# Performance work log

Measured on AMD Instinct MI355X. Metric: run time of the kernel, lower is better.

Reference implementation:

```python
import jax, jax.numpy as jnp
import numpy as np

T, S, B, D, H, FFN = 1024, 1024, 4, 1024, 16, 4096
HD = D // H
EPS = 1e-5


def xavier(key, shape, gain=1.0):
    fan_out, fan_in = shape
    a = gain * np.sqrt(6.0 / (fan_in + fan_out))
    return jax.random.uniform(key, shape, jnp.float32, -a, a)


def layer_norm(x, g, b):
    mu = jnp.mean(x, axis=-1, keepdims=True)
    var = jnp.mean(jnp.square(x - mu), axis=-1, keepdims=True)
    return (x - mu) / jnp.sqrt(var + EPS) * g + b


def mha(q, k, v, Wq, bq, Wk, bk, Wv, bv, Wo, bo, key_padding_mask=None, attn_mask=None):
    # q: [t,b,d]; k,v: [s,b,d]; key_padding_mask: [b,s] bool (True = pad)
    t, b, d = q.shape
    s = v.shape[0]
    if key_padding_mask is not None:
        # original zeroes the KEY tensor before projection
        k = k * (~key_padding_mask).T[:, :, None]
    Q = (q @ Wq.T + bq).reshape(t, b, H, HD)
    K = (k @ Wk.T + bk).reshape(s, b, H, HD)
    V = (v @ Wv.T + bv).reshape(s, b, H, HD)
    scores = jnp.einsum('tbhk,sbhk->bhts', Q, K) / jnp.sqrt(jnp.float32(HD))
    if attn_mask is not None:
        scores = scores + attn_mask  # additive [t,s] broadcast over b,h
    p = jax.nn.softmax(scores, axis=-1)
    ctx = jnp.einsum('bhts,sbhk->tbhk', p, V)  # [t,b,h,hd]
    out = ctx.reshape(t, b, d)
    attn_w = jnp.swapaxes(ctx, 0, 2)  # [h,b,t,hd] as in original
    return out @ Wo.T + bo, attn_w


def setup_inputs() -> dict:
    key = jax.random.key(0)
    ks = jax.random.split(key, 16)
    inv2 = 1.0 / np.sqrt(2.0)
    d = {
        'state': jax.random.normal(ks[0], (T, B, D), jnp.float32),
        'encoder_out': jax.random.normal(ks[1], (S, B, D), jnp.float32),
        'self_attn_mask': jnp.triu(jnp.full((T, T), -1e9, jnp.float32), 1),
        'self_attn_padding_mask': jnp.zeros((B, T), bool),
        'encoder_padding_mask': jnp.broadcast_to(jnp.arange(S)[None, :] >= (S - S // 10), (B, S)),
        # self-attention projections
        'sa_Wq': xavier(ks[2], (D, D), inv2), 'sa_bq': jnp.zeros((D,), jnp.float32),
        'sa_Wk': xavier(ks[3], (D, D), inv2), 'sa_bk': jnp.zeros((D,), jnp.float32),
        'sa_Wv': xavier(ks[4], (D, D), inv2), 'sa_bv': jnp.zeros((D,), jnp.float32),
        'sa_Wo': xavier(ks[5], (D, D)), 'sa_bo': jnp.zeros((D,), jnp.float32),
        # encoder-decoder attention projections
        'ea_Wq': xavier(ks[6], (D, D), inv2), 'ea_bq': jnp.zeros((D,), jnp.float32),
        'ea_Wk': xavier(ks[7], (D, D), inv2), 'ea_bk': jnp.zeros((D,), jnp.float32),
        'ea_Wv': xavier(ks[8], (D, D), inv2), 'ea_bv': jnp.zeros((D,), jnp.float32),
        'ea_Wo': xavier(ks[9], (D, D)), 'ea_bo': jnp.zeros((D,), jnp.float32),
        # layernorms
        'ln1_g': jnp.ones((D,), jnp.float32), 'ln1_b': jnp.zeros((D,), jnp.float32),
        'ln2_g': jnp.ones((D,), jnp.float32), 'ln2_b': jnp.zeros((D,), jnp.float32),
        'ln3_g': jnp.ones((D,), jnp.float32), 'ln3_b': jnp.zeros((D,), jnp.float32),
        # FFN
        'fc1_W': xavier(ks[10], (FFN, D)), 'fc1_b': jnp.zeros((FFN,), jnp.float32),
        'fc2_W': xavier(ks[11], (D, FFN)), 'fc2_b': jnp.zeros((D,), jnp.float32),
    }
    return d


def reference(state, encoder_out, self_attn_mask, self_attn_padding_mask, encoder_padding_mask,
              sa_Wq, sa_bq, sa_Wk, sa_bk, sa_Wv, sa_bv, sa_Wo, sa_bo,
              ea_Wq, ea_bq, ea_Wk, ea_bk, ea_Wv, ea_bv, ea_Wo, ea_bo,
              ln1_g, ln1_b, ln2_g, ln2_b, ln3_g, ln3_b,
              fc1_W, fc1_b, fc2_W, fc2_b):
    x = state
    # self-attention block (dropout is identity in eval)
    res = x
    a, _ = mha(x, x, x, sa_Wq, sa_bq, sa_Wk, sa_bk, sa_Wv, sa_bv, sa_Wo, sa_bo,
               key_padding_mask=self_attn_padding_mask, attn_mask=self_attn_mask)
    x = layer_norm(a + res, ln1_g, ln1_b)
    # encoder-decoder attention block
    res = x
    a, attn = mha(x, encoder_out, encoder_out, ea_Wq, ea_bq, ea_Wk, ea_bk, ea_Wv, ea_bv, ea_Wo, ea_bo,
                  key_padding_mask=encoder_padding_mask, attn_mask=None)
    x = layer_norm(a + res, ln2_g, ln2_b)
    # FFN block
    res = x
    h = jax.nn.relu(x @ fc1_W.T + fc1_b)
    x = layer_norm(h @ fc2_W.T + fc2_b + res, ln3_g, ln3_b)
    return (x, attn)
```

## Files before the change

kernel.cpp:

```cpp
#include <hip/hip_runtime.h>
#include <hip/hip_bf16.h>


typedef __attribute__((ext_vector_type(8))) short bf16x8;
typedef __attribute__((ext_vector_type(4))) float f32x4;
typedef __attribute__((ext_vector_type(8))) unsigned short us8;
typedef __attribute__((ext_vector_type(4))) unsigned short us4;

#define AS1 __attribute__((address_space(1)))
#define AS3 __attribute__((address_space(3)))

#define T_LEN 1024
#define S_LEN 1024
#define B_DIM 4
#define D_MOD 1024
#define H_NUM 16
#define FFN_D 4096
#define NTOK  4096

__device__ __forceinline__ float b2f(unsigned short u) {
    return __uint_as_float(((unsigned int)u) << 16);
}
__device__ __forceinline__ unsigned short f2b(float f) {
    unsigned int x = __float_as_uint(f);
    x += 0x7fffu + ((x >> 16) & 1u);
    return (unsigned short)(x >> 16);
}

struct CvtArgs {
    const float* s[12];
    unsigned short* d[12];
};

__global__ __launch_bounds__(256) void cvt_all_kernel(CvtArgs a)
{
    const int cnt[12] = {2048, 2048, 512, 512, 512, 512, 512, 512, 512, 512, 2048, 2048};
    int bid = blockIdx.x;
    int seg = 0;
    while (bid >= cnt[seg]) { bid -= cnt[seg]; ++seg; }
    const size_t off = (size_t)bid * 2048 + threadIdx.x * 8;
    const float* src = a.s[seg] + off;
    unsigned short* dst = a.d[seg] + off;
    const f32x4 v0 = *(const f32x4*)src;
    const f32x4 v1 = *(const f32x4*)(src + 4);
    us8 o;
#pragma unroll
    for (int j = 0; j < 4; ++j) { o[j] = f2b(v0[j]); o[4 + j] = f2b(v1[j]); }
    *(us8*)dst = o;
}

template <int BN>
__global__ __launch_bounds__(512, 1) void gemm8ph_kernel(
    const unsigned short* __restrict__ A,
    const unsigned short* __restrict__ W,
    const float* __restrict__ b0, const float* __restrict__ b1,
    const float* __restrict__ b2, const float* __restrict__ b3,
    const int* __restrict__ rowmask, unsigned int maskbits,
    unsigned short* __restrict__ p0, unsigned short* __restrict__ p1,
    unsigned short* __restrict__ p2, unsigned short* __restrict__ p3,
    int ostride,
    const float* __restrict__ resid, float* __restrict__ outf,
    float* __restrict__ partf,
    int M, int N, int K, int relu, int ksplit)
{
    constexpr int NR  = BN / 64;
    constexpr int BLH = (BN * 64) / 8192;
    constexpr int BBUF = BN * 128;

    __shared__ __align__(16) char ldsb[65536 + 2 * BBUF];

    const int tid  = threadIdx.x;
    const int lane = tid & 63;
    const int wid  = tid >> 6;
    const int wr   = wid >> 2;
    const int wc   = wid & 3;
    const int row0 = blockIdx.x * 256;
    const int col0 = blockIdx.y * BN;
    const int rsel = lane & 15;
    const int kg2  = (lane >> 4) * 16;
    const int kz   = blockIdx.z;
    const int Keff = K / ksplit;
    const int koff = kz * Keff;
    const int NT   = Keff >> 6;

    f32x4 acc[8][NR];
#pragma unroll
    for (int m = 0; m < 8; ++m)
#pragma unroll
        for (int n = 0; n < NR; ++n)
            acc[m][n] = (f32x4){0.f, 0.f, 0.f, 0.f};

    auto stageA = [&](int buf, int half, int t) {
        const int k0 = koff + (t << 6);
#pragma unroll
        for (int i = 0; i < 2; ++i) {
            const unsigned int beta = (unsigned int)(half * 16384 + i * 8192 + tid * 16);
            const unsigned int lam  = beta ^ (((beta >> 7) & 7u) << 4);
            const char* src = (const char*)A +
                ((size_t)(row0 + (int)(lam >> 7)) * K + k0) * 2 + (lam & 127u);
            __builtin_amdgcn_global_load_lds((const AS1 void*)src,
                (AS3 void*)(ldsb + buf * 32768 + beta), 16, 0, 0);
        }
    };
    auto stageB = [&](int buf, int half, int t) {
        const int k0 = koff + (t << 6);
#pragma unroll
        for (int i = 0; i < BLH; ++i) {
            const unsigned int beta = (unsigned int)(half * (BN * 64) + i * 8192 + tid * 16);
            const unsigned int lam  = beta ^ (((beta >> 7) & 7u) << 4);
            const char* src = (const char*)W +
                ((size_t)(col0 + (int)(lam >> 7)) * K + k0) * 2 + (lam & 127u);
            __builtin_amdgcn_global_load_lds((const AS1 void*)src,
                (AS3 void*)(ldsb + 65536 + buf * BBUF + beta), 16, 0, 0);
        }
    };
    auto readA = [&](int buf, int m, int k) -> bf16x8 {
        const int r = wr * 128 + m * 16 + rsel;
        const unsigned int l  = (unsigned int)(r * 128 + k * 64 + kg2);
        const unsigned int ph = l ^ (((unsigned int)(r & 7)) << 4);
        return *(const bf16x8*)(ldsb + buf * 32768 + ph);
    };
    auto readB = [&](int buf, int n, int k) -> bf16x8 {
        const int r = wc * (BN / 4) + n * 16 + rsel;
        const unsigned int l  = (unsigned int)(r * 128 + k * 64 + kg2);
        const unsigned int ph = l ^ (((unsigned int)(r & 7)) << 4);
        return *(const bf16x8*)(ldsb + 65536 + buf * BBUF + ph);
    };

    stageA(0, 0, 0); stageA(0, 1, 0); stageB(0, 0, 0); stageB(0, 1, 0);
    stageA(1, 0, 1); stageA(1, 1, 1);
    asm volatile("s_waitcnt vmcnt(4)" ::: "memory");
    __builtin_amdgcn_s_barrier();

    bf16x8 Afr[8][2], Bfr[NR][2];

    for (int t = 0; t < NT; ++t) {
        const int cur = t & 1;
#pragma unroll
        for (int m = 0; m < 4; ++m) { Afr[m][0] = readA(cur, m, 0); Afr[m][1] = readA(cur, m, 1); }
#pragma unroll
        for (int n = 0; n < NR; ++n) Bfr[n][0] = readB(cur, n, 0);
        if (t + 1 < NT) stageB(cur ^ 1, 0, t + 1);
        __builtin_amdgcn_s_barrier();
        asm volatile("s_waitcnt lgkmcnt(0)" ::: "memory");
        __builtin_amdgcn_sched_barrier(0);
        __builtin_amdgcn_s_setprio(1);
#pragma unroll
        for (int m = 0; m < 4; ++m)
#pragma unroll
            for (int n = 0; n < NR; ++n)
                acc[m][n] = __builtin_amdgcn_mfma_f32_16x16x32_bf16(Afr[m][0], Bfr[n][0], acc[m][n], 0, 0, 0);
        __builtin_amdgcn_s_setprio(0);
        __builtin_amdgcn_s_barrier();
#pragma unroll
        for (int m = 4; m < 8; ++m) { Afr[m][0] = readA(cur, m, 0); Afr[m][1] = readA(cur, m, 1); }
#pragma unroll
        for (int n = 0; n < NR; ++n) Bfr[n][1] = readB(cur, n, 1);
        if (t + 1 < NT) stageB(cur ^ 1, 1, t + 1);
        __builtin_amdgcn_s_barrier();
        asm volatile("s_waitcnt lgkmcnt(0)" ::: "memory");
        __builtin_amdgcn_sched_barrier(0);
        __builtin_amdgcn_s_setprio(1);
#pragma unroll
        for (int m = 4; m < 8; ++m)
#pragma unroll
            for (int n = 0; n < NR; ++n)
                acc[m][n] = __builtin_amdgcn_mfma_f32_16x16x32_bf16(Afr[m][0], Bfr[n][0], acc[m][n], 0, 0, 0);
        __builtin_amdgcn_s_setprio(0);
        __builtin_amdgcn_s_barrier();
        if (t + 2 < NT) stageA(cur, 0, t + 2);
        __builtin_amdgcn_s_barrier();
        __builtin_amdgcn_s_setprio(1);
#pragma unroll
        for (int m = 0; m < 4; ++m)
#pragma unroll
            for (int n = 0; n < NR; ++n)
                acc[m][n] = __builtin_amdgcn_mfma_f32_16x16x32_bf16(Afr[m][1], Bfr[n][1], acc[m][n], 0, 0, 0);
        __builtin_amdgcn_s_setprio(0);
        __builtin_amdgcn_s_barrier();
        if (t + 2 < NT) stageA(cur, 1, t + 2);
        __builtin_amdgcn_s_barrier();
        __builtin_amdgcn_s_setprio(1);
#pragma unroll
        for (int m = 4; m < 8; ++m)
#pragma unroll
            for (int n = 0; n < NR; ++n)
                acc[m][n] = __builtin_amdgcn_mfma_f32_16x16x32_bf16(Afr[m][1], Bfr[n][1], acc[m][n], 0, 0, 0);
        __builtin_amdgcn_s_setprio(0);
        if (t + 2 < NT) { asm volatile("s_waitcnt vmcnt(4)" ::: "memory"); }
        else            { asm volatile("s_waitcnt vmcnt(0)" ::: "memory"); }
        __builtin_amdgcn_s_barrier();
    }

    const int seq  = M >> 2;
    const int c    = col0 >> 10;
    unsigned short* op = c == 0 ? p0 : c == 1 ? p1 : c == 2 ? p2 : p3;
    const float*    bp = c == 0 ? b0 : c == 1 ? b1 : c == 2 ? b2 : b3;
    const bool um = rowmask && ((maskbits >> c) & 1u);
    const int rbas = (lane >> 4) * 4;
    if (partf && kz > 0) {
#pragma unroll
        for (int m = 0; m < 8; ++m)
#pragma unroll
            for (int n = 0; n < NR; ++n)
#pragma unroll
                for (int j = 0; j < 4; ++j) {
                    const int gr = row0 + wr * 128 + m * 16 + rbas + j;
                    const int gc = col0 + wc * (BN / 4) + n * 16 + rsel;
                    partf[(size_t)gr * N + gc] = acc[m][n][j];
                }
    } else {
#pragma unroll
        for (int m = 0; m < 8; ++m)
#pragma unroll
            for (int n = 0; n < NR; ++n)
#pragma unroll
                for (int j = 0; j < 4; ++j) {
                    const int gr = row0 + wr * 128 + m * 16 + rbas + j;
                    const int gc = col0 + wc * (BN / 4) + n * 16 + rsel;
                    float v = acc[m][n][j];
                    if (um && rowmask[(gr & 3) * seq + (gr >> 2)] != 0) v = 0.f;
                    v += bp[gc & 1023];
                    if (relu) v = fmaxf(v, 0.f);
                    if (resid) v += resid[(size_t)gr * N + gc];
                    if (outf) outf[(size_t)gr * N + gc] = v;
                    else      op[(size_t)gr * ostride + (gc & 1023)] = f2b(v);
                }
    }
}

__global__ __launch_bounds__(256) void vtrans_kernel(
    const unsigned short* __restrict__ Vb, unsigned short* __restrict__ Vt)
{
    __shared__ unsigned short tile[64 * 72];
    const int tid = threadIdx.x;
    const int t0  = blockIdx.x * 64;
    const int bh  = blockIdx.y;
    const int h   = bh & (H_NUM - 1);
    const int b   = bh >> 4;

    const int r   = tid >> 2;
    const int c16 = (tid & 3) * 16;
    const unsigned short* src = Vb + ((size_t)(t0 + r) * B_DIM + b) * D_MOD + h * 64 + c16;
    *(us8*)&tile[r * 72 + c16]     = *(const us8*)src;
    *(us8*)&tile[r * 72 + c16 + 8] = *(const us8*)(src + 8);
    __syncthreads();

    const int dr  = tid >> 2;
    const int tch = (tid & 3) * 16;
    us8 o0, o1;
#pragma unroll
    for (int j = 0; j < 8; ++j) {
        o0[j] = tile[(tch + j) * 72 + dr];
        o1[j] = tile[(tch + 8 + j) * 72 + dr];
    }
    unsigned short* dst = Vt + (size_t)(bh * 64 + dr) * S_LEN + t0 + tch;
    *(us8*)dst       = o0;
    *(us8*)(dst + 8) = o1;
}

__global__ __launch_bounds__(256, 3) void flash_mfma_kernel(
    const unsigned short* __restrict__ Qb,
    const unsigned short* __restrict__ Kb,
    const unsigned short* __restrict__ Vt,
    unsigned short* __restrict__ outc,
    float* __restrict__ outp,
    int causal)
{
    __shared__ __align__(16) unsigned short Ks[2][64 * 64];
    __shared__ __align__(16) unsigned short Vts[2][64 * 64];
    __shared__ __align__(16) unsigned short Ps[4][16 * 72];

    const int tid  = threadIdx.x;
    const int lane = tid & 63;
    const int wv   = tid >> 6;
    const int g    = lane >> 4;
    const int n    = lane & 15;
    const int t0   = blockIdx.x * 64;
    const int bh   = blockIdx.y;
    const int h    = bh & (H_NUM - 1);
    const int b    = bh >> 4;
    const int woff = wv * 16;

    bf16x8 qa[2];
    {
        const unsigned short* qptr =
            Qb + ((size_t)(t0 + woff + n) * B_DIM + b) * D_MOD + h * 64 + g * 8;
        qa[0] = *(const bf16x8*)qptr;
        qa[1] = *(const bf16x8*)(qptr + 32);
    }

    f32x4 ctx[4];
#pragma unroll
    for (int nt = 0; nt < 4; ++nt) ctx[nt] = (f32x4){0.f, 0.f, 0.f, 0.f};
    float m_run[4], l_run[4];
#pragma unroll
    for (int j = 0; j < 4; ++j) { m_run[j] = -INFINITY; l_run[j] = 0.f; }

    unsigned short* pw = &Ps[wv][0];
    const int smax = causal ? (t0 + 64) : S_LEN;
    const int NTt  = smax >> 6;

    auto stage = [&](int buf, int s0) {
#pragma unroll
        for (int i = 0; i < 2; ++i) {
            const unsigned int beta = (unsigned int)(i * 4096 + tid * 16);
            const unsigned int lam  = beta ^ (((beta >> 7) & 7u) << 4);
            const int row = (int)(lam >> 7);
            const unsigned int colb = lam & 127u;
            const char* srcK = (const char*)Kb +
                ((size_t)((s0 + row) * B_DIM + b) * D_MOD + h * 64) * 2 + colb;
            __builtin_amdgcn_global_load_lds((const AS1 void*)srcK,
                (AS3 void*)((char*)&Ks[buf][0] + beta), 16, 0, 0);
            const char* srcV = (const char*)Vt +
                ((size_t)(bh * 64 + row) * S_LEN + s0) * 2 + colb;
            __builtin_amdgcn_global_load_lds((const AS1 void*)srcV,
                (AS3 void*)((char*)&Vts[buf][0] + beta), 16, 0, 0);
        }
    };

    stage(0, 0);
    for (int t = 0; t < NTt; ++t) {
        const int s0  = t << 6;
        const int cur = t & 1;
        asm volatile("s_waitcnt vmcnt(0)" ::: "memory");
        __builtin_amdgcn_s_barrier();
        if (t + 1 < NTt) stage(cur ^ 1, s0 + 64);

        f32x4 sacc[4];
#pragma unroll
        for (int u = 0; u < 4; ++u) sacc[u] = (f32x4){0.f, 0.f, 0.f, 0.f};
#pragma unroll
        for (int u = 0; u < 4; ++u) {
#pragma unroll
            for (int kc = 0; kc < 2; ++kc) {
                const int r = u * 16 + n;
                const unsigned int l  = (unsigned int)(r * 128 + kc * 64 + g * 16);
                const unsigned int ph = l ^ (((unsigned int)(r & 7)) << 4);
                const bf16x8 kb = *(const bf16x8*)((const char*)&Ks[cur][0] + ph);
                sacc[u] = __builtin_amdgcn_mfma_f32_16x16x32_bf16(qa[kc], kb, sacc[u], 0, 0, 0);
            }
        }

        const bool diag = causal && (s0 + 64 > t0);
        float scj[4];
#pragma unroll
        for (int j = 0; j < 4; ++j) {
            float p[4];
#pragma unroll
            for (int u = 0; u < 4; ++u) p[u] = sacc[u][j] * 0.125f;
            if (diag) {
                const int tq = t0 + woff + g * 4 + j;
#pragma unroll
                for (int u = 0; u < 4; ++u)
                    if (s0 + u * 16 + n > tq) p[u] += -1e9f;
            }
            float pm = fmaxf(fmaxf(p[0], p[1]), fmaxf(p[2], p[3]));
            pm = fmaxf(pm, __shfl_xor(pm, 1));
            pm = fmaxf(pm, __shfl_xor(pm, 2));
            pm = fmaxf(pm, __shfl_xor(pm, 4));
            pm = fmaxf(pm, __shfl_xor(pm, 8));
            const float m_new = fmaxf(m_run[j], pm);
            const float sc = __expf(m_run[j] - m_new);
            m_run[j] = m_new;
            float e[4];
#pragma unroll
            for (int u = 0; u < 4; ++u) e[u] = __expf(p[u] - m_new);
            float ls = (e[0] + e[1]) + (e[2] + e[3]);
            ls += __shfl_xor(ls, 1);
            ls += __shfl_xor(ls, 2);
            ls += __shfl_xor(ls, 4);
            ls += __shfl_xor(ls, 8);
            l_run[j] = l_run[j] * sc + ls;
            scj[j] = sc;
#pragma unroll
            for (int u = 0; u < 4; ++u)
                pw[(g * 4 + j) * 72 + u * 16 + n] = f2b(e[u]);
        }
#pragma unroll
        for (int nt = 0; nt < 4; ++nt)
#pragma unroll
            for (int j = 0; j < 4; ++j) ctx[nt][j] *= scj[j];

        bf16x8 pa[2];
#pragma unroll
        for (int ks = 0; ks < 2; ++ks)
            pa[ks] = *(const bf16x8*)&pw[n * 72 + ks * 32 + g * 8];
#pragma unroll
        for (int nt = 0; nt < 4; ++nt) {
#pragma unroll
            for (int ks = 0; ks < 2; ++ks) {
                const int r = nt * 16 + n;
                const unsigned int l  = (unsigned int)(r * 128 + ks * 64 + g * 16);
                const unsigned int ph = l ^ (((unsigned int)(r & 7)) << 4);
                const bf16x8 vb = *(const bf16x8*)((const char*)&Vts[cur][0] + ph);
                ctx[nt] = __builtin_amdgcn_mfma_f32_16x16x32_bf16(pa[ks], vb, ctx[nt], 0, 0, 0);
            }
        }
    }

    float inv[4];
#pragma unroll
    for (int j = 0; j < 4; ++j) inv[j] = 1.f / l_run[j];
#pragma unroll
    for (int nt = 0; nt < 4; ++nt) {
#pragma unroll
        for (int j = 0; j < 4; ++j) {
            const int t = t0 + woff + g * 4 + j;
            const int d = nt * 16 + n;
            const float v = ctx[nt][j] * inv[j];
            outc[((size_t)t * B_DIM + b) * D_MOD + h * 64 + d] = f2b(v);
            if (outp)
                outp[((size_t)(h * B_DIM + b) * T_LEN + t) * 64 + d] = v;
        }
    }
}

__global__ __launch_bounds__(256) void layernorm_kernel(
    const float* __restrict__ y,
    const float* __restrict__ part,
    const float* __restrict__ g,
    const float* __restrict__ be,
    float* __restrict__ out_f,
    unsigned short* __restrict__ out_bf)
{
    __shared__ float red[8];
    const int row = blockIdx.x;
    const int tid = threadIdx.x;
    f32x4 v = *(const f32x4*)&y[(size_t)row * D_MOD + tid * 4];
    if (part) {
        const f32x4 pv = *(const f32x4*)&part[(size_t)row * D_MOD + tid * 4];
#pragma unroll
        for (int j = 0; j < 4; ++j) v[j] += pv[j];
    }
    float s = v[0] + v[1] + v[2] + v[3];
#pragma unroll
    for (int o = 32; o > 0; o >>= 1) s += __shfl_xor(s, o);
    if ((tid & 63) == 0) red[tid >> 6] = s;
    __syncthreads();
    const float mu = (red[0] + red[1] + red[2] + red[3]) * (1.f / D_MOD);
    const float d0 = v[0] - mu, d1 = v[1] - mu, d2 = v[2] - mu, d3 = v[3] - mu;
    float s2 = d0 * d0 + d1 * d1 + d2 * d2 + d3 * d3;
#pragma unroll
    for (int o = 32; o > 0; o >>= 1) s2 += __shfl_xor(s2, o);
    if ((tid & 63) == 0) red[4 + (tid >> 6)] = s2;
    __syncthreads();
    const float var  = (red[4] + red[5] + red[6] + red[7]) * (1.f / D_MOD);
    const float rstd = rsqrtf(var + 1e-5f);
    const float dd[4] = {d0, d1, d2, d3};
    f32x4 of;
    us4 ob;
#pragma unroll
    for (int j = 0; j < 4; ++j) {
        const int col = tid * 4 + j;
        const float r = dd[j] * rstd * g[col] + be[col];
        of[j] = r;
        ob[j] = f2b(r);
    }
    const size_t oi = (size_t)row * D_MOD + tid * 4;
    if (out_f)  *(f32x4*)&out_f[oi] = of;
    if (out_bf) *(us4*)&out_bf[oi]  = ob;
}

extern "C" void kernel_launch(void* const* d_in, const int* in_sizes, int n_in,
                              void* d_out, int out_size, void* d_ws, size_t ws_size,
                              hipStream_t stream) {
    (void)in_sizes; (void)n_in; (void)out_size; (void)ws_size;

    const float* x0    = (const float*)d_in[0];
    const float* enc   = (const float*)d_in[1];
    const int* sa_pad  = (const int*)d_in[3];
    const int* ea_pad  = (const int*)d_in[4];
    const float* sa_Wq = (const float*)d_in[5];
    const float* sa_bq = (const float*)d_in[6];
    const float* sa_Wk = (const float*)d_in[7];
    const float* sa_bk = (const float*)d_in[8];
    const float* sa_Wv = (const float*)d_in[9];
    const float* sa_bv = (const float*)d_in[10];
    const float* sa_Wo = (const float*)d_in[11];
    const float* sa_bo = (const float*)d_in[12];
    const float* ea_Wq = (const float*)d_in[13];
    const float* ea_bq = (const float*)d_in[14];
    const float* ea_Wk = (const float*)d_in[15];
    const float* ea_bk = (const float*)d_in[16];
    const float* ea_Wv = (const float*)d_in[17];
    const float* ea_bv = (const float*)d_in[18];
    const float* ea_Wo = (const float*)d_in[19];
    const float* ea_bo = (const float*)d_in[20];
    const float* ln1_g = (const float*)d_in[21];
    const float* ln1_b = (const float*)d_in[22];
    const float* ln2_g = (const float*)d_in[23];
    const float* ln2_b = (const float*)d_in[24];
    const float* ln3_g = (const float*)d_in[25];
    const float* ln3_b = (const float*)d_in[26];
    const float* fc1_W = (const float*)d_in[27];
    const float* fc1_b = (const float*)d_in[28];
    const float* fc2_W = (const float*)d_in[29];
    const float* fc2_b = (const float*)d_in[30];

    const size_t DD = (size_t)D_MOD * D_MOD;
    const size_t FD = (size_t)FFN_D * D_MOD;
    const size_t SL = (size_t)NTOK * D_MOD;

    unsigned short* ws_us = (unsigned short*)d_ws;
    unsigned short* wb[10];
    for (int i = 0; i < 8; ++i) wb[i] = ws_us + i * DD;
    wb[8] = ws_us + 8 * DD;
    wb[9] = ws_us + 8 * DD + FD;
    unsigned short* abf = ws_us + 8 * DD + 2 * FD;
    unsigned short* ebf = abf + SL;
    unsigned short* Cb  = ebf + SL;
    unsigned short* Qb  = Cb + SL;
    unsigned short* Kb  = Qb + SL;
    unsigned short* Vb  = Kb + SL;
    unsigned short* Vt  = Vb + SL;
    unsigned short* Hbf = Qb;
    float* fbase = (float*)(Vt + SL);
    float* Yf  = fbase;
    float* X1f = fbase + SL;
    float* Pq  = (float*)Qb;
    float* Pa  = (float*)abf;

    float* outx = (float*)d_out;
    float* outa = outx + SL;

    const dim3 blk(256);
    const dim3 blk512(512);
    const dim3 g_attn(T_LEN / 64, B_DIM * H_NUM);
    unsigned short* nbf = nullptr;
    float* nff = nullptr;
    const float* nf = nullptr;
    const int* ni = nullptr;

    {
        CvtArgs ca;
        const float* srcs[12]  = {x0, enc, sa_Wq, sa_Wk, sa_Wv, sa_Wo,
                                  ea_Wq, ea_Wk, ea_Wv, ea_Wo, fc1_W, fc2_W};
        unsigned short* dsts[12] = {abf, ebf, wb[0], wb[1], wb[2], wb[3],
                                    wb[4], wb[5], wb[6], wb[7], wb[8], wb[9]};
        for (int i = 0; i < 12; ++i) { ca.s[i] = srcs[i]; ca.d[i] = dsts[i]; }
        cvt_all_kernel<<<dim3(12288), blk, 0, stream>>>(ca);
    }

    gemm8ph_kernel<256><<<dim3(16, 12, 1), blk512, 0, stream>>>(
        abf, wb[0], sa_bq, sa_bk, sa_bv, sa_bv, sa_pad, 0x2u,
        Qb, Kb, Vb, Vb, D_MOD, nf, nff, nff, NTOK, 3072, D_MOD, 0, 1);
    vtrans_kernel<<<g_attn, blk, 0, stream>>>(Vb, Vt);
    flash_mfma_kernel<<<g_attn, blk, 0, stream>>>(Qb, Kb, Vt, Cb, nff, 1);
    gemm8ph_kernel<128><<<dim3(16, 8, 2), blk512, 0, stream>>>(
        Cb, wb[3], sa_bo, sa_bo, sa_bo, sa_bo, ni, 0u,
        nbf, nbf, nbf, nbf, D_MOD, x0, Yf, Pq, NTOK, D_MOD, D_MOD, 0, 2);
    layernorm_kernel<<<dim3(NTOK), blk, 0, stream>>>(Yf, Pq, ln1_g, ln1_b, X1f, abf);

    gemm8ph_kernel<128><<<dim3(16, 8, 1), blk512, 0, stream>>>(
        abf, wb[4], ea_bq, ea_bq, ea_bq, ea_bq, ni, 0u,
        Qb, Qb, Qb, Qb, D_MOD, nf, nff, nff, NTOK, D_MOD, D_MOD, 0, 1);
    gemm8ph_kernel<128><<<dim3(16, 16, 1), blk512, 0, stream>>>(
        ebf, wb[5], ea_bk, ea_bv, ea_bv, ea_bv, ea_pad, 0x1u,
        Kb, Vb, Vb, Vb, D_MOD, nf, nff, nff, NTOK, 2048, D_MOD, 0, 1);
    vtrans_kernel<<<g_attn, blk, 0, stream>>>(Vb, Vt);
    flash_mfma_kernel<<<g_attn, blk, 0, stream>>>(Qb, Kb, Vt, Cb, outa, 0);
    gemm8ph_kernel<128><<<dim3(16, 8, 2), blk512, 0, stream>>>(
        Cb, wb[7], ea_bo, ea_bo, ea_bo, ea_bo, ni, 0u,
        nbf, nbf, nbf, nbf, D_MOD, X1f, Yf, Pq, NTOK, D_MOD, D_MOD, 0, 2);
    layernorm_kernel<<<dim3(NTOK), blk, 0, stream>>>(Yf, Pq, ln2_g, ln2_b, X1f, ebf);

    gemm8ph_kernel<256><<<dim3(16, 16, 1), blk512, 0, stream>>>(
        ebf, wb[8], fc1_b, fc1_b + 1024, fc1_b + 2048, fc1_b + 3072, ni, 0u,
        Hbf, Hbf + 1024, Hbf + 2048, Hbf + 3072, FFN_D, nf, nff, nff,
        NTOK, FFN_D, D_MOD, 1, 1);
    gemm8ph_kernel<128><<<dim3(16, 8, 2), blk512, 0, stream>>>(
        Hbf, wb[9], fc2_b, fc2_b, fc2_b, fc2_b, ni, 0u,
        nbf, nbf, nbf, nbf, D_MOD, X1f, Yf, Pa, NTOK, D_MOD, FFN_D, 0, 2);
    layernorm_kernel<<<dim3(NTOK), blk, 0, stream>>>(Yf, Pa, ln3_g, ln3_b, outx, nbf);
}
```

Before: 683.6 us.

## Transpose flash-attention score MFMA, simplify softmax reductions, add NR=2 GEMM schedule

```diff
diff --git a/kernel.cpp b/kernel.cpp
--- a/kernel.cpp
+++ b/kernel.cpp
@@ -132,64 +132,102 @@
     asm volatile("s_waitcnt vmcnt(4)" ::: "memory");
     __builtin_amdgcn_s_barrier();
 
-    bf16x8 Afr[8][2], Bfr[NR][2];
-
-    for (int t = 0; t < NT; ++t) {
-        const int cur = t & 1;
-#pragma unroll
-        for (int m = 0; m < 4; ++m) { Afr[m][0] = readA(cur, m, 0); Afr[m][1] = readA(cur, m, 1); }
-#pragma unroll
-        for (int n = 0; n < NR; ++n) Bfr[n][0] = readB(cur, n, 0);
-        if (t + 1 < NT) stageB(cur ^ 1, 0, t + 1);
-        __builtin_amdgcn_s_barrier();
-        asm volatile("s_waitcnt lgkmcnt(0)" ::: "memory");
-        __builtin_amdgcn_sched_barrier(0);
-        __builtin_amdgcn_s_setprio(1);
-#pragma unroll
-        for (int m = 0; m < 4; ++m)
-#pragma unroll
-            for (int n = 0; n < NR; ++n)
-                acc[m][n] = __builtin_amdgcn_mfma_f32_16x16x32_bf16(Afr[m][0], Bfr[n][0], acc[m][n], 0, 0, 0);
-        __builtin_amdgcn_s_setprio(0);
-        __builtin_amdgcn_s_barrier();
-#pragma unroll
-        for (int m = 4; m < 8; ++m) { Afr[m][0] = readA(cur, m, 0); Afr[m][1] = readA(cur, m, 1); }
-#pragma unroll
-        for (int n = 0; n < NR; ++n) Bfr[n][1] = readB(cur, n, 1);
-        if (t + 1 < NT) stageB(cur ^ 1, 1, t + 1);
-        __builtin_amdgcn_s_barrier();
-        asm volatile("s_waitcnt lgkmcnt(0)" ::: "memory");
-        __builtin_amdgcn_sched_barrier(0);
-        __builtin_amdgcn_s_setprio(1);
-#pragma unroll
-        for (int m = 4; m < 8; ++m)
-#pragma unroll
-            for (int n = 0; n < NR; ++n)
-                acc[m][n] = __builtin_amdgcn_mfma_f32_16x16x32_bf16(Afr[m][0], Bfr[n][0], acc[m][n], 0, 0, 0);
-        __builtin_amdgcn_s_setprio(0);
-        __builtin_amdgcn_s_barrier();
-        if (t + 2 < NT) stageA(cur, 0, t + 2);
-        __builtin_amdgcn_s_barrier();
-        __builtin_amdgcn_s_setprio(1);
-#pragma unroll
-        for (int m = 0; m < 4; ++m)
-#pragma unroll
-            for (int n = 0; n < NR; ++n)
-                acc[m][n] = __builtin_amdgcn_mfma_f32_16x16x32_bf16(Afr[m][1], Bfr[n][1], acc[m][n], 0, 0, 0);
-        __builtin_amdgcn_s_setprio(0);
-        __builtin_amdgcn_s_barrier();
-        if (t + 2 < NT) stageA(cur, 1, t + 2);
-        __builtin_amdgcn_s_barrier();
-        __builtin_amdgcn_s_setprio(1);
-#pragma unroll
-        for (int m = 4; m < 8; ++m)
-#pragma unroll
-            for (int n = 0; n < NR; ++n)
-                acc[m][n] = __builtin_amdgcn_mfma_f32_16x16x32_bf16(Afr[m][1], Bfr[n][1], acc[m][n], 0, 0, 0);
-        __builtin_amdgcn_s_setprio(0);
-        if (t + 2 < NT) { asm volatile("s_waitcnt vmcnt(4)" ::: "memory"); }
-        else            { asm volatile("s_waitcnt vmcnt(0)" ::: "memory"); }
-        __builtin_amdgcn_s_barrier();
+    if constexpr (NR == 2) {
+        bf16x8 Af[8][2], Bf[2][2];
+        for (int t = 0; t < NT; ++t) {
+            const int cur = t & 1;
+#pragma unroll
+            for (int m = 0; m < 8; ++m) { Af[m][0] = readA(cur, m, 0); Af[m][1] = readA(cur, m, 1); }
+#pragma unroll
+            for (int n = 0; n < 2; ++n) Bf[n][0] = readB(cur, n, 0);
+            if (t + 1 < NT) { stageB(cur ^ 1, 0, t + 1); stageB(cur ^ 1, 1, t + 1); }
+            __builtin_amdgcn_s_barrier();
+            asm volatile("s_waitcnt lgkmcnt(0)" ::: "memory");
+            __builtin_amdgcn_sched_barrier(0);
+            __builtin_amdgcn_s_setprio(1);
+#pragma unroll
+            for (int m = 0; m < 8; ++m)
+#pragma unroll
+                for (int n = 0; n < 2; ++n)
+                    acc[m][n] = __builtin_amdgcn_mfma_f32_16x16x32_bf16(Af[m][0], Bf[n][0], acc[m][n], 0, 0, 0);
+            __builtin_amdgcn_s_setprio(0);
+            __builtin_amdgcn_s_barrier();
+#pragma unroll
+            for (int n = 0; n < 2; ++n) Bf[n][1] = readB(cur, n, 1);
+            if (t + 2 < NT) { stageA(cur, 0, t + 2); stageA(cur, 1, t + 2); }
+            __builtin_amdgcn_s_barrier();
+            asm volatile("s_waitcnt lgkmcnt(0)" ::: "memory");
+            __builtin_amdgcn_sched_barrier(0);
+            __builtin_amdgcn_s_setprio(1);
+#pragma unroll
+            for (int m = 0; m < 8; ++m)
+#pragma unroll
+                for (int n = 0; n < 2; ++n)
+                    acc[m][n] = __builtin_amdgcn_mfma_f32_16x16x32_bf16(Af[m][1], Bf[n][1], acc[m][n], 0, 0, 0);
+            __builtin_amdgcn_s_setprio(0);
+            if (t + 2 < NT) { asm volatile("s_waitcnt vmcnt(4)" ::: "memory"); }
+            else            { asm volatile("s_waitcnt vmcnt(0)" ::: "memory"); }
+            __builtin_amdgcn_s_barrier();
+        }
+    } else {
+        bf16x8 Afr[8][2], Bfr[NR][2];
+        for (int t = 0; t < NT; ++t) {
+            const int cur = t & 1;
+#pragma unroll
+            for (int m = 0; m < 4; ++m) { Afr[m][0] = readA(cur, m, 0); Afr[m][1] = readA(cur, m, 1); }
+#pragma unroll
+            for (int n = 0; n < NR; ++n) Bfr[n][0] = readB(cur, n, 0);
+            if (t + 1 < NT) stageB(cur ^ 1, 0, t + 1);
+            __builtin_amdgcn_s_barrier();
+            asm volatile("s_waitcnt lgkmcnt(0)" ::: "memory");
+            __builtin_amdgcn_sched_barrier(0);
+            __builtin_amdgcn_s_setprio(1);
+#pragma unroll
+            for (int m = 0; m < 4; ++m)
+#pragma unroll
+                for (int n = 0; n < NR; ++n)
+                    acc[m][n] = __builtin_amdgcn_mfma_f32_16x16x32_bf16(Afr[m][0], Bfr[n][0], acc[m][n], 0, 0, 0);
+            __builtin_amdgcn_s_setprio(0);
+            __builtin_amdgcn_s_barrier();
+#pragma unroll
+            for (int m = 4; m < 8; ++m) { Afr[m][0] = readA(cur, m, 0); Afr[m][1] = readA(cur, m, 1); }
+#pragma unroll
+            for (int n = 0; n < NR; ++n) Bfr[n][1] = readB(cur, n, 1);
+            if (t + 1 < NT) stageB(cur ^ 1, 1, t + 1);
+            __builtin_amdgcn_s_barrier();
+            asm volatile("s_waitcnt lgkmcnt(0)" ::: "memory");
+            __builtin_amdgcn_sched_barrier(0);
+            __builtin_amdgcn_s_setprio(1);
+#pragma unroll
+            for (int m = 4; m < 8; ++m)
+#pragma unroll
+                for (int n = 0; n < NR; ++n)
+                    acc[m][n] = __builtin_amdgcn_mfma_f32_16x16x32_bf16(Afr[m][0], Bfr[n][0], acc[m][n], 0, 0, 0);
+            __builtin_amdgcn_s_setprio(0);
+            __builtin_amdgcn_s_barrier();
+            if (t + 2 < NT) stageA(cur, 0, t + 2);
+            __builtin_amdgcn_s_barrier();
+            __builtin_amdgcn_s_setprio(1);
+#pragma unroll
+            for (int m = 0; m < 4; ++m)
+#pragma unroll
+                for (int n = 0; n < NR; ++n)
+                    acc[m][n] = __builtin_amdgcn_mfma_f32_16x16x32_bf16(Afr[m][1], Bfr[n][1], acc[m][n], 0, 0, 0);
+            __builtin_amdgcn_s_setprio(0);
+            __builtin_amdgcn_s_barrier();
+            if (t + 2 < NT) stageA(cur, 1, t + 2);
+            __builtin_amdgcn_s_barrier();
+            __builtin_amdgcn_s_setprio(1);
+#pragma unroll
+            for (int m = 4; m < 8; ++m)
+#pragma unroll
+                for (int n = 0; n < NR; ++n)
+                    acc[m][n] = __builtin_amdgcn_mfma_f32_16x16x32_bf16(Afr[m][1], Bfr[n][1], acc[m][n], 0, 0, 0);
+            __builtin_amdgcn_s_setprio(0);
+            if (t + 2 < NT) { asm volatile("s_waitcnt vmcnt(4)" ::: "memory"); }
+            else            { asm volatile("s_waitcnt vmcnt(0)" ::: "memory"); }
+            __builtin_amdgcn_s_barrier();
+        }
     }
 
     const int seq  = M >> 2;
@@ -234,8 +272,8 @@
 {
     __shared__ unsigned short tile[64 * 72];
     const int tid = threadIdx.x;
-    const int t0  = blockIdx.x * 64;
-    const int bh  = blockIdx.y;
+    const int bh  = blockIdx.x;
+    const int t0  = blockIdx.y * 64;
     const int h   = bh & (H_NUM - 1);
     const int b   = bh >> 4;
 
@@ -276,8 +314,9 @@
     const int wv   = tid >> 6;
     const int g    = lane >> 4;
     const int n    = lane & 15;
-    const int t0   = blockIdx.x * 64;
-    const int bh   = blockIdx.y;
+    const int g4   = g * 4;
+    const int bh   = blockIdx.x;
+    const int t0   = blockIdx.y * 64;
     const int h    = bh & (H_NUM - 1);
     const int b    = bh >> 4;
     const int woff = wv * 16;
@@ -293,13 +332,12 @@
     f32x4 ctx[4];
 #pragma unroll
     for (int nt = 0; nt < 4; ++nt) ctx[nt] = (f32x4){0.f, 0.f, 0.f, 0.f};
-    float m_run[4], l_run[4];
-#pragma unroll
-    for (int j = 0; j < 4; ++j) { m_run[j] = -INFINITY; l_run[j] = 0.f; }
+    float m_run = -INFINITY, l_run = 0.f;
 
     unsigned short* pw = &Ps[wv][0];
     const int smax = causal ? (t0 + 64) : S_LEN;
     const int NTt  = smax >> 6;
+    const int tq   = t0 + woff + n;
 
     auto stage = [&](int buf, int s0) {
 #pragma unroll
@@ -338,49 +376,51 @@
                 const unsigned int l  = (unsigned int)(r * 128 + kc * 64 + g * 16);
                 const unsigned int ph = l ^ (((unsigned int)(r & 7)) << 4);
                 const bf16x8 kb = *(const bf16x8*)((const char*)&Ks[cur][0] + ph);
-                sacc[u] = __builtin_amdgcn_mfma_f32_16x16x32_bf16(qa[kc], kb, sacc[u], 0, 0, 0);
+                sacc[u] = __builtin_amdgcn_mfma_f32_16x16x32_bf16(kb, qa[kc], sacc[u], 0, 0, 0);
             }
         }
 
         const bool diag = causal && (s0 + 64 > t0);
-        float scj[4];
-#pragma unroll
-        for (int j = 0; j < 4; ++j) {
-            float p[4];
-#pragma unroll
-            for (int u = 0; u < 4; ++u) p[u] = sacc[u][j] * 0.125f;
-            if (diag) {
-                const int tq = t0 + woff + g * 4 + j;
-#pragma unroll
-                for (int u = 0; u < 4; ++u)
-                    if (s0 + u * 16 + n > tq) p[u] += -1e9f;
+        float pv[4][4];
+        float pm = -INFINITY;
+#pragma unroll
+        for (int u = 0; u < 4; ++u)
+#pragma unroll
+            for (int j = 0; j < 4; ++j) {
+                float p = sacc[u][j] * 0.125f;
+                if (diag && (s0 + u * 16 + g4 + j > tq)) p += -1e9f;
+                pv[u][j] = p;
+                pm = fmaxf(pm, p);
             }
-            float pm = fmaxf(fmaxf(p[0], p[1]), fmaxf(p[2], p[3]));
-            pm = fmaxf(pm, __shfl_xor(pm, 1));
-            pm = fmaxf(pm, __shfl_xor(pm, 2));
-            pm = fmaxf(pm, __shfl_xor(pm, 4));
-            pm = fmaxf(pm, __shfl_xor(pm, 8));
-            const float m_new = fmaxf(m_run[j], pm);
-            const float sc = __expf(m_run[j] - m_new);
-            m_run[j] = m_new;
-            float e[4];
-#pragma unroll
-            for (int u = 0; u < 4; ++u) e[u] = __expf(p[u] - m_new);
-            float ls = (e[0] + e[1]) + (e[2] + e[3]);
-            ls += __shfl_xor(ls, 1);
-            ls += __shfl_xor(ls, 2);
-            ls += __shfl_xor(ls, 4);
-            ls += __shfl_xor(ls, 8);
-            l_run[j] = l_run[j] * sc + ls;
-            scj[j] = sc;
-#pragma unroll
-            for (int u = 0; u < 4; ++u)
-                pw[(g * 4 + j) * 72 + u * 16 + n] = f2b(e[u]);
-        }
+        pm = fmaxf(pm, __shfl_xor(pm, 16));
+        pm = fmaxf(pm, __shfl_xor(pm, 32));
+        const float m_new = fmaxf(m_run, pm);
+        const float sc = __expf(m_run - m_new);
+        m_run = m_new;
+        float ls = 0.f;
+#pragma unroll
+        for (int u = 0; u < 4; ++u) {
+            const float e0 = __expf(pv[u][0] - m_new);
+            const float e1 = __expf(pv[u][1] - m_new);
+            const float e2 = __expf(pv[u][2] - m_new);
+            const float e3 = __expf(pv[u][3] - m_new);
+            ls += (e0 + e1) + (e2 + e3);
+            const unsigned int w0 = (unsigned int)f2b(e0) | ((unsigned int)f2b(e1) << 16);
+            const unsigned int w1 = (unsigned int)f2b(e2) | ((unsigned int)f2b(e3) << 16);
+            *(unsigned int*)&pw[n * 72 + u * 16 + g4]     = w0;
+            *(unsigned int*)&pw[n * 72 + u * 16 + g4 + 2] = w1;
+        }
+        ls += __shfl_xor(ls, 16);
+        ls += __shfl_xor(ls, 32);
+        l_run = l_run * sc + ls;
+
+        float scq[4];
+#pragma unroll
+        for (int j = 0; j < 4; ++j) scq[j] = __shfl(sc, g4 + j);
 #pragma unroll
         for (int nt = 0; nt < 4; ++nt)
 #pragma unroll
-            for (int j = 0; j < 4; ++j) ctx[nt][j] *= scj[j];
+            for (int j = 0; j < 4; ++j) ctx[nt][j] *= scq[j];
 
         bf16x8 pa[2];
 #pragma unroll
@@ -399,16 +439,16 @@
         }
     }
 
-    float inv[4];
-#pragma unroll
-    for (int j = 0; j < 4; ++j) inv[j] = 1.f / l_run[j];
+    float invq[4];
+#pragma unroll
+    for (int j = 0; j < 4; ++j) invq[j] = 1.f / __shfl(l_run, g4 + j);
 #pragma unroll
     for (int nt = 0; nt < 4; ++nt) {
 #pragma unroll
         for (int j = 0; j < 4; ++j) {
-            const int t = t0 + woff + g * 4 + j;
+            const int t = t0 + woff + g4 + j;
             const int d = nt * 16 + n;
-            const float v = ctx[nt][j] * inv[j];
+            const float v = ctx[nt][j] * invq[j];
             outc[((size_t)t * B_DIM + b) * D_MOD + h * 64 + d] = f2b(v);
             if (outp)
                 outp[((size_t)(h * B_DIM + b) * T_LEN + t) * 64 + d] = v;
@@ -526,7 +566,7 @@
 
     const dim3 blk(256);
     const dim3 blk512(512);
-    const dim3 g_attn(T_LEN / 64, B_DIM * H_NUM);
+    const dim3 g_attn(B_DIM * H_NUM, T_LEN / 64);
     unsigned short* nbf = nullptr;
     float* nff = nullptr;
     const float* nf = nullptr;
```

After: 619.2 us. 9.4% less time.
